# Optimization experiments

Hardware: AMD Instinct MI355X
Metric: run time of the kernel (lower is better)

The kernel has to match this reference:

```python
import jax, jax.numpy as jnp
import numpy as np

N_NODES = 50000
N_EDGES = 800000
C_IN = 64
HID = 3
C_OUT = 128
ATTR = 6


def setup_inputs() -> dict:
    key = jax.random.key(0)
    ks = jax.random.split(key, 16)
    inp = {
        "x": jax.random.normal(ks[0], (N_NODES, C_IN), dtype=jnp.float32),
        "edge_index0": jax.random.randint(ks[1], (2, N_EDGES), 0, N_NODES, dtype=jnp.int32).astype(jnp.int64),
        "edge_attr0": jax.random.normal(ks[2], (N_EDGES, ATTR), dtype=jnp.float32),
        "edge_index1": jax.random.randint(ks[3], (2, N_EDGES), 0, N_NODES, dtype=jnp.int32).astype(jnp.int64),
        "edge_attr1": jax.random.normal(ks[4], (N_EDGES, ATTR), dtype=jnp.float32),
        "W_in0": jax.random.normal(ks[5], (ATTR, HID * C_IN), dtype=jnp.float32) * 0.1,
        "b_in0": jax.random.normal(ks[6], (HID * C_IN,), dtype=jnp.float32) * 0.1,
        "W_out0": jax.random.normal(ks[7], (HID * C_IN, C_OUT), dtype=jnp.float32) * 0.05,
        "b_out0": jax.random.normal(ks[8], (C_OUT,), dtype=jnp.float32) * 0.05,
        "W_in1": jax.random.normal(ks[9], (ATTR, HID * C_IN), dtype=jnp.float32) * 0.1,
        "b_in1": jax.random.normal(ks[10], (HID * C_IN,), dtype=jnp.float32) * 0.1,
        "W_out1": jax.random.normal(ks[11], (HID * C_IN, C_OUT), dtype=jnp.float32) * 0.05,
        "b_out1": jax.random.normal(ks[12], (C_OUT,), dtype=jnp.float32) * 0.05,
    }
    return inp


def _spatial_graph_conv(x, edge_index, edge_attr, W_in, b_in, W_out, b_out):
    # PyG MessagePassing default flow: x_j = x[edge_index[0]] (source),
    # aggregate (add) at edge_index[1] (target).
    src, dst = edge_index[0], edge_index[1]
    n_nodes, c_in = x.shape
    x_j = x[src]                                   # [E, C]
    scaling = jax.nn.relu(edge_attr @ W_in + b_in)  # [E, 3C]
    n_edges = x_j.shape[0]
    msg = (scaling.reshape(n_edges, c_in, -1) * x_j[:, :, None]).reshape(n_edges, -1)  # [E, 3C]
    aggr = jax.ops.segment_sum(msg, dst, num_segments=n_nodes)  # [N, 3C]
    return jnp.tanh(aggr @ W_out + b_out)  # [N, C_OUT]; dropout p=0 -> identity


def reference(x, edge_index0, edge_attr0, edge_index1, edge_attr1,
              W_in0, b_in0, W_out0, b_out0, W_in1, b_in1, W_out1, b_out1):
    # aGCN_conv with use_A=2: two independent SpatialGraphConv layers, concat on feature dim.
    y0 = _spatial_graph_conv(x, edge_index0, edge_attr0, W_in0, b_in0, W_out0, b_out0)
    y1 = _spatial_graph_conv(x, edge_index1, edge_attr1, W_in1, b_in1, W_out1, b_out1)
    return jnp.concatenate([y0, y1], axis=1)  # [N, 2*C_OUT]
```

## Files before the change

### kernel.cpp

```cpp
#include <hip/hip_runtime.h>

#define N_NODES 50000
#define N_EDGES 800000
#define C_IN 64
#define HID 3
#define C_OUTC 128
#define ATTR 6
#define K3 192
#define NBK 782
#define NPAD 50048
#define CAP 1280
#define CAPP 1472
#define EPB 4096
#define P1B 196
#define AGS 200

typedef _Float16 half4v __attribute__((ext_vector_type(4)));
typedef _Float16 half8  __attribute__((ext_vector_type(8)));
typedef float    floatx4 __attribute__((ext_vector_type(4)));

#define RFL(x) __builtin_amdgcn_readfirstlane((int)(x))

static __device__ __forceinline__ float lo16f(unsigned v) {
    unsigned short s = (unsigned short)(v & 0xFFFF);
    _Float16 h;
    __builtin_memcpy(&h, &s, 2);
    return (float)h;
}
static __device__ __forceinline__ float hi16f(unsigned v) { return lo16f(v >> 16); }

static __device__ __forceinline__ unsigned pkh(float a, float b) {
    _Float16 ha = (_Float16)a, hb = (_Float16)b;
    unsigned short xa, xbits;
    __builtin_memcpy(&xa, &ha, 2);
    __builtin_memcpy(&xbits, &hb, 2);
    return (unsigned)xa | ((unsigned)xbits << 16);
}

__global__ __launch_bounds__(512)
void pass1(const int* __restrict__ ei0, const int* __restrict__ ei1,
           int* __restrict__ cursor, int2* __restrict__ seg)
{
    __shared__ int s_cnt[NBK], s_ofs[NBK], s_pos[NBK], s_gbase[NBK];
    __shared__ int2 st_es[EPB];
    __shared__ unsigned short st_b[EPB];
    __shared__ int wsum[8];
    const int t = threadIdx.x, lane = t & 63, wid = t >> 6;
    const int l = (blockIdx.x >= P1B) ? 1 : 0;
    const int* ei = l ? ei1 : ei0;
    const int base = (blockIdx.x - l * P1B) * EPB;

    for (int i = t; i < NBK; i += 512) s_cnt[i] = 0;
    __syncthreads();

    int src[8], dst[8];
    const int e0 = base + t * 8;
    if (e0 + 7 < N_EDGES) {
        const int4 s0 = *(const int4*)(ei + e0);
        const int4 s1 = *(const int4*)(ei + e0 + 4);
        const int4 d0 = *(const int4*)(ei + N_EDGES + e0);
        const int4 d1 = *(const int4*)(ei + N_EDGES + e0 + 4);
        src[0]=s0.x; src[1]=s0.y; src[2]=s0.z; src[3]=s0.w;
        src[4]=s1.x; src[5]=s1.y; src[6]=s1.z; src[7]=s1.w;
        dst[0]=d0.x; dst[1]=d0.y; dst[2]=d0.z; dst[3]=d0.w;
        dst[4]=d1.x; dst[5]=d1.y; dst[6]=d1.z; dst[7]=d1.w;
    } else {
#pragma unroll
        for (int j = 0; j < 8; ++j) {
            const int e = e0 + j;
            if (e < N_EDGES) { src[j] = ei[e]; dst[j] = ei[N_EDGES + e]; }
            else dst[j] = -1;
        }
    }
#pragma unroll
    for (int j = 0; j < 8; ++j)
        if (dst[j] >= 0) atomicAdd(&s_cnt[dst[j] >> 6], 1);
    __syncthreads();

    const int i0 = 2 * t, i1 = 2 * t + 1;
    const int v0 = (i0 < NBK) ? s_cnt[i0] : 0;
    const int v1 = (i1 < NBK) ? s_cnt[i1] : 0;
    const int pv = v0 + v1;
    int incl = pv;
#pragma unroll
    for (int off = 1; off < 64; off <<= 1) {
        const int u = __shfl_up(incl, off, 64);
        if (lane >= off) incl += u;
    }
    if (lane == 63) wsum[wid] = incl;
    __syncthreads();
    if (wid == 0) {
        int s = (lane < 8) ? wsum[lane] : 0;
#pragma unroll
        for (int off = 1; off < 8; off <<= 1) {
            const int u = __shfl_up(s, off, 64);
            if (lane >= off) s += u;
        }
        if (lane < 8) wsum[lane] = s;
    }
    __syncthreads();
    const int ex = (wid ? wsum[wid - 1] : 0) + (incl - pv);
    if (i0 < NBK) { s_ofs[i0] = ex;      s_pos[i0] = ex; }
    if (i1 < NBK) { s_ofs[i1] = ex + v0; s_pos[i1] = ex + v0; }
    __syncthreads();

    for (int i = t; i < NBK; i += 512)
        s_gbase[i] = atomicAdd(&cursor[(l << 10) + i], s_cnt[i]);

#pragma unroll
    for (int j = 0; j < 8; ++j) {
        if (dst[j] >= 0) {
            const int b = dst[j] >> 6;
            const int p = atomicAdd(&s_pos[b], 1);
            st_es[p] = make_int2((e0 + j) | ((dst[j] & 63) << 20), src[j]);
            st_b[p]  = (unsigned short)b;
        }
    }
    __syncthreads();

    const int total = (N_EDGES - base < EPB) ? (N_EDGES - base) : EPB;
    for (int j = t; j < total; j += 512) {
        const int b = st_b[j];
        const int g = s_gbase[b] + (j - s_ofs[b]);
        if (g < CAP) seg[(size_t)(l * NBK + b) * CAP + g] = st_es[j];
    }
}

__global__ __launch_bounds__(256)
void pass2(const int* __restrict__ cursor, const int2* __restrict__ seg,
           const float* __restrict__ ea0, const float* __restrict__ ea1,
           int4* __restrict__ csr, int2* __restrict__ row_info)
{
    __shared__ int hist[64], cur[64], pex[64];
    const int t = threadIdx.x;
    const int l = (blockIdx.x >= NBK) ? 1 : 0;
    const int fb = blockIdx.x - l * NBK;
    const float* __restrict__ ea = l ? ea1 : ea0;
    const int S0 = cursor[(l << 10) + fb];
    const int S = (S0 < CAP) ? S0 : CAP;
    const size_t segbase = (size_t)(l * NBK + fb) * CAP;
    const size_t base = (size_t)(l * NBK + fb) * CAPP;
    const int2* segb = seg + segbase;

    if (t < 64) hist[t] = 0;
    __syncthreads();
    for (int i = t; i < S; i += 256)
        atomicAdd(&hist[(segb[i].x >> 20) & 63], 1);
    __syncthreads();

    if (t < 64) {
        const int v = hist[t];
        const int pv = (v + 3) & ~3;
        int incl = pv;
#pragma unroll
        for (int off = 1; off < 64; off <<= 1) {
            const int u = __shfl_up(incl, off, 64);
            if (t >= off) incl += u;
        }
        const int excl = incl - pv;
        cur[t] = excl;
        pex[t] = excl;
        const int node = fb * 64 + t;
        if (node < N_NODES)
            row_info[l * NPAD + node] = make_int2((int)base + excl, v);
    }
    __syncthreads();

    for (int i = t; i < S; i += 256) {
        const int2 p = segb[i];
        const int dl = (p.x >> 20) & 63;
        const int eid = p.x & 0xFFFFF;
        const float2 q01 = *(const float2*)(ea + (size_t)eid * ATTR + 0);
        const float2 q23 = *(const float2*)(ea + (size_t)eid * ATTR + 2);
        const float2 q45 = *(const float2*)(ea + (size_t)eid * ATTR + 4);
        const int pos = atomicAdd(&cur[dl], 1);
        int4 ent;
        ent.x = p.y;
        ent.y = (int)pkh(q01.x, q01.y);
        ent.z = (int)pkh(q23.x, q23.y);
        ent.w = (int)pkh(q45.x, q45.y);
        csr[base + pos] = ent;
    }

    if (t < 64) {
        const int v = hist[t];
        const int pv = (v + 3) & ~3;
        for (int p = pex[t] + v; p < pex[t] + pv; ++p)
            csr[base + p] = make_int4(N_NODES, 0, 0, 0);
    }
}

#define XW4 ((N_NODES * C_IN) / 4)
#define XW4Z (((N_NODES + 1) * C_IN) / 4)
__global__ __launch_bounds__(256)
void xcvt(const float* __restrict__ x, unsigned short* __restrict__ xb)
{
    const int i = blockIdx.x * 256 + threadIdx.x;
    if (i < XW4) {
        const float4 v = ((const float4*)x)[i];
        ushort4 o;
        unsigned u;
        u = __float_as_uint(v.x); o.x = (unsigned short)((u + 0x7FFF + ((u >> 16) & 1)) >> 16);
        u = __float_as_uint(v.y); o.y = (unsigned short)((u + 0x7FFF + ((u >> 16) & 1)) >> 16);
        u = __float_as_uint(v.z); o.z = (unsigned short)((u + 0x7FFF + ((u >> 16) & 1)) >> 16);
        u = __float_as_uint(v.w); o.w = (unsigned short)((u + 0x7FFF + ((u >> 16) & 1)) >> 16);
        ((ushort4*)xb)[i] = o;
    } else if (i < XW4Z) {
        ((ushort4*)xb)[i] = make_ushort4(0, 0, 0, 0);
    }
}

__global__ __launch_bounds__(256)
void wcvt(const float* __restrict__ Wo0, const float* __restrict__ Wo1,
          _Float16* __restrict__ w16)
{
    const int i = blockIdx.x * 256 + threadIdx.x;
    if (i < 2 * K3 * C_OUTC) {
        const int layer = i / (K3 * C_OUTC), r = i % (K3 * C_OUTC);
        const int k = r / C_OUTC, n = r % C_OUTC;
        const float v = (layer ? Wo1 : Wo0)[r];
        w16[((size_t)layer * (K3 / 8) + (k >> 3)) * C_OUTC * 8 + n * 8 + (k & 7)] =
            (_Float16)v;
    }
}

#define EDGE_FMA(P0, P1, P2, HJ)                                               \
    {                                                                          \
        const float xv = __uint_as_float((unsigned)(HJ) << 16);                \
        const float A0 = lo16f(P0), A1 = hi16f(P0);                            \
        const float A2 = lo16f(P1), A3 = hi16f(P1);                            \
        const float A4 = lo16f(P2), A5 = hi16f(P2);                            \
        float s0 = bb[0], s1 = bb[1], s2 = bb[2];                              \
        s0 = fmaf(A0, w[0][0], s0); s1 = fmaf(A0, w[0][1], s1); s2 = fmaf(A0, w[0][2], s2); \
        s0 = fmaf(A1, w[1][0], s0); s1 = fmaf(A1, w[1][1], s1); s2 = fmaf(A1, w[1][2], s2); \
        s0 = fmaf(A2, w[2][0], s0); s1 = fmaf(A2, w[2][1], s1); s2 = fmaf(A2, w[2][2], s2); \
        s0 = fmaf(A3, w[3][0], s0); s1 = fmaf(A3, w[3][1], s1); s2 = fmaf(A3, w[3][2], s2); \
        s0 = fmaf(A4, w[4][0], s0); s1 = fmaf(A4, w[4][1], s1); s2 = fmaf(A4, w[4][2], s2); \
        s0 = fmaf(A5, w[5][0], s0); s1 = fmaf(A5, w[5][1], s1); s2 = fmaf(A5, w[5][2], s2); \
        acc0 = fmaf(fmaxf(s0, 0.f), xv, acc0);                                 \
        acc1 = fmaf(fmaxf(s1, 0.f), xv, acc1);                                 \
        acc2 = fmaf(fmaxf(s2, 0.f), xv, acc2);                                 \
    }

__global__ __launch_bounds__(256, 3)
void mega(const unsigned short* __restrict__ xb,
          const float* __restrict__ Wi0, const float* __restrict__ bi0,
          const float* __restrict__ bo0,
          const float* __restrict__ Wi1, const float* __restrict__ bi1,
          const float* __restrict__ bo1,
          const _Float16* __restrict__ w16,
          const int2* __restrict__ row_info, const int4* __restrict__ csr,
          float* __restrict__ out)
{
    __shared__ __attribute__((aligned(16))) _Float16 agg[32 * AGS];
    const int t = threadIdx.x, lane = t & 63, wv = t >> 6;
    const int l = (blockIdx.x >= 2 * NBK) ? 1 : 0;
    const int hb = blockIdx.x - l * 2 * NBK;
    const int b = hb >> 1, half = hb & 1;
    const int nodebase = b * 64 + half * 32;
    const float* Wi = l ? Wi1 : Wi0;
    const float* bi = l ? bi1 : bi0;
    const float* bo = l ? bo1 : bo0;

    const int col = 3 * lane;
    float w[ATTR][HID], bb[HID];
#pragma unroll
    for (int k = 0; k < ATTR; ++k)
#pragma unroll
        for (int h = 0; h < HID; ++h)
            w[k][h] = Wi[k * K3 + col + h];
#pragma unroll
    for (int h = 0; h < HID; ++h) bb[h] = bi[col + h];

    int2 ri = make_int2(0, 0);
    const int nd = nodebase + wv * 8 + lane;
    if (lane < 8 && nd < N_NODES) ri = row_info[l * NPAD + nd];
    const int riX = ri.x, riY = ri.y;

#pragma unroll 1
    for (int u = 0; u < 8; ++u) {
        const int cnt = RFL(__shfl(riY, u));
        const int dl = wv * 8 + u;
        _Float16* ap = &agg[dl * AGS + col];
        if (cnt == 0) {
            ap[0] = (_Float16)0.f; ap[1] = (_Float16)0.f; ap[2] = (_Float16)0.f;
            continue;
        }
        const int rb = RFL(__shfl(riX, u));
        const int nch = (cnt + 3) >> 2;
        const int4* __restrict__ ep = csr + rb;

        float acc0 = 0.f, acc1 = 0.f, acc2 = 0.f;

        int4 f0 = ep[0], f1 = ep[1], f2 = ep[2], f3 = ep[3];
        int s0_ = RFL(f0.x); unsigned p00 = RFL(f0.y), p01 = RFL(f0.z), p02 = RFL(f0.w);
        int s1_ = RFL(f1.x); unsigned p10 = RFL(f1.y), p11 = RFL(f1.z), p12 = RFL(f1.w);
        int s2_ = RFL(f2.x); unsigned p20 = RFL(f2.y), p21 = RFL(f2.z), p22 = RFL(f2.w);
        int s3_ = RFL(f3.x); unsigned p30 = RFL(f3.y), p31 = RFL(f3.z), p32 = RFL(f3.w);
        unsigned short hv0 = xb[(size_t)(unsigned)s0_ * C_IN + lane];
        unsigned short hv1 = xb[(size_t)(unsigned)s1_ * C_IN + lane];
        unsigned short hv2 = xb[(size_t)(unsigned)s2_ * C_IN + lane];
        unsigned short hv3 = xb[(size_t)(unsigned)s3_ * C_IN + lane];

#pragma unroll 1
        for (int c = 1; c < nch; ++c) {
            const int4 g0 = ep[4 * c + 0], g1 = ep[4 * c + 1];
            const int4 g2 = ep[4 * c + 2], g3 = ep[4 * c + 3];
            EDGE_FMA(p00, p01, p02, hv0);
            EDGE_FMA(p10, p11, p12, hv1);
            EDGE_FMA(p20, p21, p22, hv2);
            EDGE_FMA(p30, p31, p32, hv3);
            s0_ = RFL(g0.x); p00 = RFL(g0.y); p01 = RFL(g0.z); p02 = RFL(g0.w);
            s1_ = RFL(g1.x); p10 = RFL(g1.y); p11 = RFL(g1.z); p12 = RFL(g1.w);
            s2_ = RFL(g2.x); p20 = RFL(g2.y); p21 = RFL(g2.z); p22 = RFL(g2.w);
            s3_ = RFL(g3.x); p30 = RFL(g3.y); p31 = RFL(g3.z); p32 = RFL(g3.w);
            hv0 = xb[(size_t)(unsigned)s0_ * C_IN + lane];
            hv1 = xb[(size_t)(unsigned)s1_ * C_IN + lane];
            hv2 = xb[(size_t)(unsigned)s2_ * C_IN + lane];
            hv3 = xb[(size_t)(unsigned)s3_ * C_IN + lane];
        }
        EDGE_FMA(p00, p01, p02, hv0);
        EDGE_FMA(p10, p11, p12, hv1);
        EDGE_FMA(p20, p21, p22, hv2);
        EDGE_FMA(p30, p31, p32, hv3);

        ap[0] = (_Float16)acc0; ap[1] = (_Float16)acc1; ap[2] = (_Float16)acc2;
    }
    __syncthreads();

    const int r0 = (wv >> 1) * 16;
    const int c0 = (wv & 1) * 64;
    const int lr = lane & 15, kg = lane >> 4;
    const _Float16* __restrict__ wb = w16 + (size_t)l * (K3 / 8) * C_OUTC * 8;

    floatx4 acc[4];
#pragma unroll
    for (int nt = 0; nt < 4; ++nt) acc[nt] = (floatx4){0.f, 0.f, 0.f, 0.f};

#pragma unroll
    for (int ks = 0; ks < 6; ++ks) {
        const int kb = ks * 32;
        const half8 a = *(const half8*)(&agg[(r0 + lr) * AGS + kb + kg * 8]);
#pragma unroll
        for (int nt = 0; nt < 4; ++nt) {
            const int n = c0 + nt * 16 + lr;
            const half8 bf = *(const half8*)(wb + ((size_t)(ks * 4 + kg) * C_OUTC + n) * 8);
            acc[nt] = __builtin_amdgcn_mfma_f32_16x16x32_f16(a, bf, acc[nt], 0, 0, 0);
        }
    }

#pragma unroll
    for (int nt = 0; nt < 4; ++nt) {
        const int n = c0 + nt * 16 + lr;
        const float bv = bo[n];
#pragma unroll
        for (int r = 0; r < 4; ++r) {
            const int node = nodebase + r0 + kg * 4 + r;
            if (node < N_NODES)
                out[(size_t)node * (2 * C_OUTC) + l * C_OUTC + n] =
                    tanhf(acc[nt][r] + bv);
        }
    }
}

extern "C" void kernel_launch(void* const* d_in, const int* in_sizes, int n_in,
                              void* d_out, int out_size, void* d_ws, size_t ws_size,
                              hipStream_t stream) {
    const float* x   = (const float*)d_in[0];
    const int*   ei0 = (const int*)d_in[1];
    const float* ea0 = (const float*)d_in[2];
    const int*   ei1 = (const int*)d_in[3];
    const float* ea1 = (const float*)d_in[4];
    const float* Wi0 = (const float*)d_in[5];
    const float* bi0 = (const float*)d_in[6];
    const float* Wo0 = (const float*)d_in[7];
    const float* bo0 = (const float*)d_in[8];
    const float* Wi1 = (const float*)d_in[9];
    const float* bi1 = (const float*)d_in[10];
    const float* Wo1 = (const float*)d_in[11];
    const float* bo1 = (const float*)d_in[12];
    float* out = (float*)d_out;

    int*  cursor   = (int*)d_ws;
    int2* row_info = (int2*)(cursor + 2048);
    unsigned short* xb = (unsigned short*)(row_info + 2 * NPAD);
    int2* seg      = (int2*)(xb + (size_t)(N_NODES + 1) * C_IN);
    int4* csr      = (int4*)(seg + (size_t)2 * NBK * CAP);
    _Float16* w16  = (_Float16*)(csr + (size_t)2 * NBK * CAPP);

    hipMemsetAsync(cursor, 0, 2048 * sizeof(int), stream);
    xcvt<<<(XW4Z + 255) / 256, 256, 0, stream>>>(x, xb);
    wcvt<<<(2 * K3 * C_OUTC + 255) / 256, 256, 0, stream>>>(Wo0, Wo1, w16);
    pass1<<<2 * P1B, 512, 0, stream>>>(ei0, ei1, cursor, seg);
    pass2<<<2 * NBK, 256, 0, stream>>>(cursor, seg, ea0, ea1, csr, row_info);
    mega<<<4 * NBK, 256, 0, stream>>>(xb,
                                      Wi0, bi0, bo0,
                                      Wi1, bi1, bo1,
                                      w16, row_info, csr, out);
}
```

Before: 295.1 us.

## Fuse CSR build pass into aggregation kernel with 32-node buckets and early attr packing

```diff
diff --git a/kernel.cpp b/kernel.cpp
--- a/kernel.cpp
+++ b/kernel.cpp
@@ -7,15 +7,14 @@
 #define C_OUTC 128
 #define ATTR 6
 #define K3 192
-#define NBK 782
-#define NPAD 50048
-#define CAP 1280
-#define CAPP 1472
-#define EPB 4096
-#define P1B 196
+#define NREAL 1563
+#define NBK2 1564
+#define CAP2 768
+#define EPB2 2048
+#define P1B2 391
 #define AGS 200
-
-typedef _Float16 half4v __attribute__((ext_vector_type(4)));
+#define SORTCAP (CAP2 + 96)
+
 typedef _Float16 half8  __attribute__((ext_vector_type(8)));
 typedef float    floatx4 __attribute__((ext_vector_type(4)));
 
@@ -39,48 +38,66 @@
 
 __global__ __launch_bounds__(512)
 void pass1(const int* __restrict__ ei0, const int* __restrict__ ei1,
-           int* __restrict__ cursor, int2* __restrict__ seg)
+           const float* __restrict__ ea0, const float* __restrict__ ea1,
+           int* __restrict__ cursor, int4* __restrict__ seg)
 {
-    __shared__ int s_cnt[NBK], s_ofs[NBK], s_pos[NBK], s_gbase[NBK];
-    __shared__ int2 st_es[EPB];
-    __shared__ unsigned short st_b[EPB];
+    __shared__ int s_cnt[NBK2], s_ofs[NBK2], s_pos[NBK2], s_gbase[NBK2];
+    __shared__ int4 st_es[EPB2];
+    __shared__ unsigned short st_b[EPB2];
     __shared__ int wsum[8];
     const int t = threadIdx.x, lane = t & 63, wid = t >> 6;
-    const int l = (blockIdx.x >= P1B) ? 1 : 0;
+    const int l = (blockIdx.x >= P1B2) ? 1 : 0;
     const int* ei = l ? ei1 : ei0;
-    const int base = (blockIdx.x - l * P1B) * EPB;
-
-    for (int i = t; i < NBK; i += 512) s_cnt[i] = 0;
-    __syncthreads();
-
-    int src[8], dst[8];
-    const int e0 = base + t * 8;
-    if (e0 + 7 < N_EDGES) {
+    const float* __restrict__ ea = l ? ea1 : ea0;
+    const int base = (blockIdx.x - l * P1B2) * EPB2;
+
+    for (int i = t; i < NBK2; i += 512) s_cnt[i] = 0;
+    __syncthreads();
+
+    int src[4], dst[4];
+    unsigned pa0[4], pa1[4], pa2[4];
+    const int e0 = base + t * 4;
+    if (e0 + 3 < N_EDGES) {
         const int4 s0 = *(const int4*)(ei + e0);
-        const int4 s1 = *(const int4*)(ei + e0 + 4);
         const int4 d0 = *(const int4*)(ei + N_EDGES + e0);
-        const int4 d1 = *(const int4*)(ei + N_EDGES + e0 + 4);
         src[0]=s0.x; src[1]=s0.y; src[2]=s0.z; src[3]=s0.w;
-        src[4]=s1.x; src[5]=s1.y; src[6]=s1.z; src[7]=s1.w;
         dst[0]=d0.x; dst[1]=d0.y; dst[2]=d0.z; dst[3]=d0.w;
-        dst[4]=d1.x; dst[5]=d1.y; dst[6]=d1.z; dst[7]=d1.w;
+#pragma unroll
+        for (int j = 0; j < 4; ++j) {
+            const float2 q01 = *(const float2*)(ea + (size_t)(e0 + j) * ATTR + 0);
+            const float2 q23 = *(const float2*)(ea + (size_t)(e0 + j) * ATTR + 2);
+            const float2 q45 = *(const float2*)(ea + (size_t)(e0 + j) * ATTR + 4);
+            pa0[j] = pkh(q01.x, q01.y);
+            pa1[j] = pkh(q23.x, q23.y);
+            pa2[j] = pkh(q45.x, q45.y);
+        }
     } else {
 #pragma unroll
-        for (int j = 0; j < 8; ++j) {
+        for (int j = 0; j < 4; ++j) {
             const int e = e0 + j;
-            if (e < N_EDGES) { src[j] = ei[e]; dst[j] = ei[N_EDGES + e]; }
-            else dst[j] = -1;
-        }
-    }
-#pragma unroll
-    for (int j = 0; j < 8; ++j)
-        if (dst[j] >= 0) atomicAdd(&s_cnt[dst[j] >> 6], 1);
-    __syncthreads();
-
-    const int i0 = 2 * t, i1 = 2 * t + 1;
-    const int v0 = (i0 < NBK) ? s_cnt[i0] : 0;
-    const int v1 = (i1 < NBK) ? s_cnt[i1] : 0;
-    const int pv = v0 + v1;
+            if (e < N_EDGES) {
+                src[j] = ei[e]; dst[j] = ei[N_EDGES + e];
+                const float2 q01 = *(const float2*)(ea + (size_t)e * ATTR + 0);
+                const float2 q23 = *(const float2*)(ea + (size_t)e * ATTR + 2);
+                const float2 q45 = *(const float2*)(ea + (size_t)e * ATTR + 4);
+                pa0[j] = pkh(q01.x, q01.y);
+                pa1[j] = pkh(q23.x, q23.y);
+                pa2[j] = pkh(q45.x, q45.y);
+            } else dst[j] = -1;
+        }
+    }
+#pragma unroll
+    for (int j = 0; j < 4; ++j)
+        if (dst[j] >= 0) atomicAdd(&s_cnt[dst[j] >> 5], 1);
+    __syncthreads();
+
+    int v0 = 0, v1 = 0, v2 = 0, v3 = 0;
+    const bool hasq = (t < NBK2 / 4);
+    if (hasq) {
+        v0 = s_cnt[4 * t + 0]; v1 = s_cnt[4 * t + 1];
+        v2 = s_cnt[4 * t + 2]; v3 = s_cnt[4 * t + 3];
+    }
+    const int pv = v0 + v1 + v2 + v3;
     int incl = pv;
 #pragma unroll
     for (int off = 1; off < 64; off <<= 1) {
@@ -100,93 +117,34 @@
     }
     __syncthreads();
     const int ex = (wid ? wsum[wid - 1] : 0) + (incl - pv);
-    if (i0 < NBK) { s_ofs[i0] = ex;      s_pos[i0] = ex; }
-    if (i1 < NBK) { s_ofs[i1] = ex + v0; s_pos[i1] = ex + v0; }
-    __syncthreads();
-
-    for (int i = t; i < NBK; i += 512)
-        s_gbase[i] = atomicAdd(&cursor[(l << 10) + i], s_cnt[i]);
-
-#pragma unroll
-    for (int j = 0; j < 8; ++j) {
+    if (hasq) {
+        s_ofs[4 * t + 0] = ex;                s_pos[4 * t + 0] = ex;
+        s_ofs[4 * t + 1] = ex + v0;           s_pos[4 * t + 1] = ex + v0;
+        s_ofs[4 * t + 2] = ex + v0 + v1;      s_pos[4 * t + 2] = ex + v0 + v1;
+        s_ofs[4 * t + 3] = ex + v0 + v1 + v2; s_pos[4 * t + 3] = ex + v0 + v1 + v2;
+    }
+    __syncthreads();
+
+    for (int i = t; i < NBK2; i += 512)
+        if (s_cnt[i]) s_gbase[i] = atomicAdd(&cursor[l * NBK2 + i], s_cnt[i]);
+
+#pragma unroll
+    for (int j = 0; j < 4; ++j) {
         if (dst[j] >= 0) {
-            const int b = dst[j] >> 6;
+            const int b = dst[j] >> 5;
             const int p = atomicAdd(&s_pos[b], 1);
-            st_es[p] = make_int2((e0 + j) | ((dst[j] & 63) << 20), src[j]);
+            st_es[p] = make_int4(src[j] | ((dst[j] & 31) << 16),
+                                 (int)pa0[j], (int)pa1[j], (int)pa2[j]);
             st_b[p]  = (unsigned short)b;
         }
     }
     __syncthreads();
 
-    const int total = (N_EDGES - base < EPB) ? (N_EDGES - base) : EPB;
+    const int total = (N_EDGES - base < EPB2) ? (N_EDGES - base) : EPB2;
     for (int j = t; j < total; j += 512) {
         const int b = st_b[j];
         const int g = s_gbase[b] + (j - s_ofs[b]);
-        if (g < CAP) seg[(size_t)(l * NBK + b) * CAP + g] = st_es[j];
-    }
-}
-
-__global__ __launch_bounds__(256)
-void pass2(const int* __restrict__ cursor, const int2* __restrict__ seg,
-           const float* __restrict__ ea0, const float* __restrict__ ea1,
-           int4* __restrict__ csr, int2* __restrict__ row_info)
-{
-    __shared__ int hist[64], cur[64], pex[64];
-    const int t = threadIdx.x;
-    const int l = (blockIdx.x >= NBK) ? 1 : 0;
-    const int fb = blockIdx.x - l * NBK;
-    const float* __restrict__ ea = l ? ea1 : ea0;
-    const int S0 = cursor[(l << 10) + fb];
-    const int S = (S0 < CAP) ? S0 : CAP;
-    const size_t segbase = (size_t)(l * NBK + fb) * CAP;
-    const size_t base = (size_t)(l * NBK + fb) * CAPP;
-    const int2* segb = seg + segbase;
-
-    if (t < 64) hist[t] = 0;
-    __syncthreads();
-    for (int i = t; i < S; i += 256)
-        atomicAdd(&hist[(segb[i].x >> 20) & 63], 1);
-    __syncthreads();
-
-    if (t < 64) {
-        const int v = hist[t];
-        const int pv = (v + 3) & ~3;
-        int incl = pv;
-#pragma unroll
-        for (int off = 1; off < 64; off <<= 1) {
-            const int u = __shfl_up(incl, off, 64);
-            if (t >= off) incl += u;
-        }
-        const int excl = incl - pv;
-        cur[t] = excl;
-        pex[t] = excl;
-        const int node = fb * 64 + t;
-        if (node < N_NODES)
-            row_info[l * NPAD + node] = make_int2((int)base + excl, v);
-    }
-    __syncthreads();
-
-    for (int i = t; i < S; i += 256) {
-        const int2 p = segb[i];
-        const int dl = (p.x >> 20) & 63;
-        const int eid = p.x & 0xFFFFF;
-        const float2 q01 = *(const float2*)(ea + (size_t)eid * ATTR + 0);
-        const float2 q23 = *(const float2*)(ea + (size_t)eid * ATTR + 2);
-        const float2 q45 = *(const float2*)(ea + (size_t)eid * ATTR + 4);
-        const int pos = atomicAdd(&cur[dl], 1);
-        int4 ent;
-        ent.x = p.y;
-        ent.y = (int)pkh(q01.x, q01.y);
-        ent.z = (int)pkh(q23.x, q23.y);
-        ent.w = (int)pkh(q45.x, q45.y);
-        csr[base + pos] = ent;
-    }
-
-    if (t < 64) {
-        const int v = hist[t];
-        const int pv = (v + 3) & ~3;
-        for (int p = pex[t] + v; p < pex[t] + pv; ++p)
-            csr[base + p] = make_int4(N_NODES, 0, 0, 0);
+        if (g < CAP2) seg[(size_t)(l * NREAL + b) * CAP2 + g] = st_es[j];
     }
 }
 
@@ -242,22 +200,23 @@
         acc2 = fmaf(fmaxf(s2, 0.f), xv, acc2);                                 \
     }
 
-__global__ __launch_bounds__(256, 3)
+__global__ __launch_bounds__(256, 6)
 void mega(const unsigned short* __restrict__ xb,
           const float* __restrict__ Wi0, const float* __restrict__ bi0,
           const float* __restrict__ bo0,
           const float* __restrict__ Wi1, const float* __restrict__ bi1,
           const float* __restrict__ bo1,
           const _Float16* __restrict__ w16,
-          const int2* __restrict__ row_info, const int4* __restrict__ csr,
+          const int* __restrict__ cursor, const int4* __restrict__ seg,
           float* __restrict__ out)
 {
+    __shared__ __attribute__((aligned(16))) int4 sorted[SORTCAP];
     __shared__ __attribute__((aligned(16))) _Float16 agg[32 * AGS];
+    __shared__ int hist[32], cur[32], pex[32];
     const int t = threadIdx.x, lane = t & 63, wv = t >> 6;
-    const int l = (blockIdx.x >= 2 * NBK) ? 1 : 0;
-    const int hb = blockIdx.x - l * 2 * NBK;
-    const int b = hb >> 1, half = hb & 1;
-    const int nodebase = b * 64 + half * 32;
+    const int l = (blockIdx.x >= NREAL) ? 1 : 0;
+    const int bk = blockIdx.x - l * NREAL;
+    const int nodebase = bk * 32;
     const float* Wi = l ? Wi1 : Wi0;
     const float* bi = l ? bi1 : bi0;
     const float* bo = l ? bo1 : bo0;
@@ -272,31 +231,70 @@
 #pragma unroll
     for (int h = 0; h < HID; ++h) bb[h] = bi[col + h];
 
-    int2 ri = make_int2(0, 0);
-    const int nd = nodebase + wv * 8 + lane;
-    if (lane < 8 && nd < N_NODES) ri = row_info[l * NPAD + nd];
-    const int riX = ri.x, riY = ri.y;
+    const int S0 = cursor[l * NBK2 + bk];
+    const int S = (S0 < CAP2) ? S0 : CAP2;
+    const int4* __restrict__ segb = seg + (size_t)(l * NREAL + bk) * CAP2;
+
+    if (t < 32) hist[t] = 0;
+    __syncthreads();
+
+    int4 r0 = make_int4(0, 0, 0, 0), r1 = r0, r2 = r0;
+    const bool h0 = (t < S), h1 = (t + 256 < S), h2 = (t + 512 < S);
+    if (h0) r0 = segb[t];
+    if (h1) r1 = segb[t + 256];
+    if (h2) r2 = segb[t + 512];
+    if (h0) atomicAdd(&hist[(r0.x >> 16) & 31], 1);
+    if (h1) atomicAdd(&hist[(r1.x >> 16) & 31], 1);
+    if (h2) atomicAdd(&hist[(r2.x >> 16) & 31], 1);
+    __syncthreads();
+
+    if (t < 32) {
+        const int v = hist[t];
+        const int pvv = (v + 3) & ~3;
+        int incl = pvv;
+#pragma unroll
+        for (int off = 1; off < 32; off <<= 1) {
+            const int u = __shfl_up(incl, off, 64);
+            if (t >= off) incl += u;
+        }
+        cur[t] = incl - pvv;
+        pex[t] = incl - pvv;
+    }
+    __syncthreads();
+
+    if (h0) sorted[atomicAdd(&cur[(r0.x >> 16) & 31], 1)] = r0;
+    if (h1) sorted[atomicAdd(&cur[(r1.x >> 16) & 31], 1)] = r1;
+    if (h2) sorted[atomicAdd(&cur[(r2.x >> 16) & 31], 1)] = r2;
+    if (t < 32) {
+        const int v = hist[t], pvv = (v + 3) & ~3;
+        for (int p = pex[t] + v; p < pex[t] + pvv; ++p)
+            sorted[p] = make_int4(N_NODES, 0, 0, 0);
+    }
+    __syncthreads();
+
+    int cx = 0, px = 0;
+    if (lane < 8) { cx = hist[wv * 8 + lane]; px = pex[wv * 8 + lane]; }
 
 #pragma unroll 1
     for (int u = 0; u < 8; ++u) {
-        const int cnt = RFL(__shfl(riY, u));
+        const int cnt = RFL(__shfl(cx, u));
         const int dl = wv * 8 + u;
         _Float16* ap = &agg[dl * AGS + col];
         if (cnt == 0) {
             ap[0] = (_Float16)0.f; ap[1] = (_Float16)0.f; ap[2] = (_Float16)0.f;
             continue;
         }
-        const int rb = RFL(__shfl(riX, u));
+        const int base = RFL(__shfl(px, u));
         const int nch = (cnt + 3) >> 2;
-        const int4* __restrict__ ep = csr + rb;
+        const int4* __restrict__ ep = &sorted[base];
 
         float acc0 = 0.f, acc1 = 0.f, acc2 = 0.f;
 
         int4 f0 = ep[0], f1 = ep[1], f2 = ep[2], f3 = ep[3];
-        int s0_ = RFL(f0.x); unsigned p00 = RFL(f0.y), p01 = RFL(f0.z), p02 = RFL(f0.w);
-        int s1_ = RFL(f1.x); unsigned p10 = RFL(f1.y), p11 = RFL(f1.z), p12 = RFL(f1.w);
-        int s2_ = RFL(f2.x); unsigned p20 = RFL(f2.y), p21 = RFL(f2.z), p22 = RFL(f2.w);
-        int s3_ = RFL(f3.x); unsigned p30 = RFL(f3.y), p31 = RFL(f3.z), p32 = RFL(f3.w);
+        int s0_ = f0.x & 0xFFFF; unsigned p00 = f0.y, p01 = f0.z, p02 = f0.w;
+        int s1_ = f1.x & 0xFFFF; unsigned p10 = f1.y, p11 = f1.z, p12 = f1.w;
+        int s2_ = f2.x & 0xFFFF; unsigned p20 = f2.y, p21 = f2.z, p22 = f2.w;
+        int s3_ = f3.x & 0xFFFF; unsigned p30 = f3.y, p31 = f3.z, p32 = f3.w;
         unsigned short hv0 = xb[(size_t)(unsigned)s0_ * C_IN + lane];
         unsigned short hv1 = xb[(size_t)(unsigned)s1_ * C_IN + lane];
         unsigned short hv2 = xb[(size_t)(unsigned)s2_ * C_IN + lane];
@@ -310,10 +308,10 @@
             EDGE_FMA(p10, p11, p12, hv1);
             EDGE_FMA(p20, p21, p22, hv2);
             EDGE_FMA(p30, p31, p32, hv3);
-            s0_ = RFL(g0.x); p00 = RFL(g0.y); p01 = RFL(g0.z); p02 = RFL(g0.w);
-            s1_ = RFL(g1.x); p10 = RFL(g1.y); p11 = RFL(g1.z); p12 = RFL(g1.w);
-            s2_ = RFL(g2.x); p20 = RFL(g2.y); p21 = RFL(g2.z); p22 = RFL(g2.w);
-            s3_ = RFL(g3.x); p30 = RFL(g3.y); p31 = RFL(g3.z); p32 = RFL(g3.w);
+            s0_ = g0.x & 0xFFFF; p00 = g0.y; p01 = g0.z; p02 = g0.w;
+            s1_ = g1.x & 0xFFFF; p10 = g1.y; p11 = g1.z; p12 = g1.w;
+            s2_ = g2.x & 0xFFFF; p20 = g2.y; p21 = g2.z; p22 = g2.w;
+            s3_ = g3.x & 0xFFFF; p30 = g3.y; p31 = g3.z; p32 = g3.w;
             hv0 = xb[(size_t)(unsigned)s0_ * C_IN + lane];
             hv1 = xb[(size_t)(unsigned)s1_ * C_IN + lane];
             hv2 = xb[(size_t)(unsigned)s2_ * C_IN + lane];
@@ -328,7 +326,7 @@
     }
     __syncthreads();
 
-    const int r0 = (wv >> 1) * 16;
+    const int r0r = (wv >> 1) * 16;
     const int c0 = (wv & 1) * 64;
     const int lr = lane & 15, kg = lane >> 4;
     const _Float16* __restrict__ wb = w16 + (size_t)l * (K3 / 8) * C_OUTC * 8;
@@ -340,7 +338,7 @@
 #pragma unroll
     for (int ks = 0; ks < 6; ++ks) {
         const int kb = ks * 32;
-        const half8 a = *(const half8*)(&agg[(r0 + lr) * AGS + kb + kg * 8]);
+        const half8 a = *(const half8*)(&agg[(r0r + lr) * AGS + kb + kg * 8]);
 #pragma unroll
         for (int nt = 0; nt < 4; ++nt) {
             const int n = c0 + nt * 16 + lr;
@@ -355,7 +353,7 @@
         const float bv = bo[n];
 #pragma unroll
         for (int r = 0; r < 4; ++r) {
-            const int node = nodebase + r0 + kg * 4 + r;
+            const int node = nodebase + r0r + kg * 4 + r;
             if (node < N_NODES)
                 out[(size_t)node * (2 * C_OUTC) + l * C_OUTC + n] =
                     tanhf(acc[nt][r] + bv);
@@ -381,20 +379,17 @@
     const float* bo1 = (const float*)d_in[12];
     float* out = (float*)d_out;
 
-    int*  cursor   = (int*)d_ws;
-    int2* row_info = (int2*)(cursor + 2048);
-    unsigned short* xb = (unsigned short*)(row_info + 2 * NPAD);
-    int2* seg      = (int2*)(xb + (size_t)(N_NODES + 1) * C_IN);
-    int4* csr      = (int4*)(seg + (size_t)2 * NBK * CAP);
-    _Float16* w16  = (_Float16*)(csr + (size_t)2 * NBK * CAPP);
-
-    hipMemsetAsync(cursor, 0, 2048 * sizeof(int), stream);
+    int* cursor        = (int*)d_ws;
+    unsigned short* xb = (unsigned short*)(cursor + 2 * NBK2);
+    int4* seg          = (int4*)(xb + (size_t)(N_NODES + 1) * C_IN);
+    _Float16* w16      = (_Float16*)(seg + (size_t)2 * NREAL * CAP2);
+
+    hipMemsetAsync(cursor, 0, 2 * NBK2 * sizeof(int), stream);
     xcvt<<<(XW4Z + 255) / 256, 256, 0, stream>>>(x, xb);
     wcvt<<<(2 * K3 * C_OUTC + 255) / 256, 256, 0, stream>>>(Wo0, Wo1, w16);
-    pass1<<<2 * P1B, 512, 0, stream>>>(ei0, ei1, cursor, seg);
-    pass2<<<2 * NBK, 256, 0, stream>>>(cursor, seg, ea0, ea1, csr, row_info);
-    mega<<<4 * NBK, 256, 0, stream>>>(xb,
-                                      Wi0, bi0, bo0,
-                                      Wi1, bi1, bo1,
-                                      w16, row_info, csr, out);
-}
+    pass1<<<2 * P1B2, 512, 0, stream>>>(ei0, ei1, ea0, ea1, cursor, seg);
+    mega<<<2 * NREAL, 256, 0, stream>>>(xb,
+                                        Wi0, bi0, bo0,
+                                        Wi1, bi1, bo1,
+                                        w16, cursor, seg, out);
+}
```

Measured after the change: 276.1 us. 6.4% less time.
